# Optimization experiments

Hardware: AMD Instinct MI355X
Metric: run time of the kernel (lower is better)

Reference implementation:

```python
import jax, jax.numpy as jnp
import numpy as np

H = 16      # n_heads
HD = 48     # head_dim
D = H * HD  # d_model = 768
DZ = 128    # pair dim
EPS = 1e-5


def setup_inputs() -> dict:
    key = jax.random.key(0)
    ks = jax.random.split(key, 12)
    B, S = 1, 1024
    sc = 0.02
    return {
        "s": jax.random.normal(ks[0], (B, S, D), jnp.float32),
        "z": jax.random.normal(ks[1], (B, S, S, DZ), jnp.float32),
        "Wq": jax.random.normal(ks[2], (D, D), jnp.float32) * sc,
        "bq": jax.random.normal(ks[3], (D,), jnp.float32) * sc,
        "Wk": jax.random.normal(ks[4], (D, D), jnp.float32) * sc,
        "Wv": jax.random.normal(ks[5], (D, D), jnp.float32) * sc,
        "Wg": jax.random.normal(ks[6], (D, D), jnp.float32) * sc,
        "ln_w": jnp.ones((DZ,), jnp.float32),
        "ln_b": jnp.zeros((DZ,), jnp.float32),
        "Wz": jax.random.normal(ks[7], (H, DZ), jnp.float32) * sc,
        "Wo": jax.random.normal(ks[8], (D, D), jnp.float32) * sc,
    }


def reference(s, z, Wq, bq, Wk, Wv, Wg, ln_w, ln_b, Wz, Wo):
    B, S, _ = s.shape
    # fused QKV projection (q has bias; k, v do not)
    q = (s @ Wq.T + bq).reshape(B, S, H, HD).transpose(0, 2, 1, 3)  # [B,H,S,hd]
    k = (s @ Wk.T).reshape(B, S, H, HD).transpose(0, 2, 1, 3)
    v = (s @ Wv.T).reshape(B, S, H, HD).transpose(0, 2, 1, 3)
    # pair bias: LayerNorm(z) then Linear(DZ -> H), used as additive attn bias
    mu = jnp.mean(z, axis=-1, keepdims=True)
    var = jnp.mean(jnp.square(z - mu), axis=-1, keepdims=True)
    zn = (z - mu) * jax.lax.rsqrt(var + EPS) * ln_w + ln_b
    bias = jnp.einsum('bstc,hc->bhst', zn, Wz)  # [B,H,S,S]
    # scaled dot-product attention with pair bias
    scores = jnp.einsum('bhsd,bhtd->bhst', q, k) * (HD ** -0.5) + bias
    a = jax.nn.softmax(scores, axis=-1)
    o = jnp.einsum('bhst,bhtd->bhsd', a, v)           # [B,H,S,hd]
    o = o.transpose(0, 2, 1, 3).reshape(B, S, D)      # [B,S,D]
    # sigmoid gating and output projection
    g = s @ Wg.T
    o = o * jax.nn.sigmoid(g)
    return o @ Wo.T
```

## Files before the change

kernel.cpp:

```cpp
#include <hip/hip_runtime.h>

constexpr int H  = 16;
constexpr int HD = 48;
constexpr int D  = 768;
constexpr int DZ = 128;
constexpr int S  = 1024;
constexpr float EPS = 1e-5f;

typedef __attribute__((ext_vector_type(8))) short bf16x8;
typedef __attribute__((ext_vector_type(4))) float f32x4;

__device__ __forceinline__ float sigmoidf_(float x) { return 1.f / (1.f + __expf(-x)); }

__device__ __forceinline__ unsigned short f2b(float f) {
  unsigned u = __float_as_uint(f);
  u += 0x7FFFu + ((u >> 16) & 1u);
  return (unsigned short)(u >> 16);
}
__device__ __forceinline__ float b2f(unsigned short u) {
  return __uint_as_float((unsigned)u << 16);
}
__device__ __forceinline__ void split2(float x, unsigned short& h, unsigned short& l) {
  const unsigned short hb = f2b(x);
  const float hf = __uint_as_float((unsigned)hb << 16);
  h = hb;
  l = f2b(x - hf);
}
__device__ __forceinline__ unsigned pack2(unsigned short a, unsigned short b) {
  return (unsigned)a | ((unsigned)b << 16);
}

__global__ __launch_bounds__(256)
void prep_kernel(const float* __restrict__ s, const float* __restrict__ Wq,
                 const float* __restrict__ Wk, const float* __restrict__ Wv,
                 const float* __restrict__ Wg, const float* __restrict__ Wo,
                 unsigned short* __restrict__ s_hi,
                 unsigned short* __restrict__ w_hi, unsigned short* __restrict__ w_lo,
                 const float* __restrict__ Wz, const float* __restrict__ ln_w,
                 const float* __restrict__ ln_b, unsigned short* __restrict__ wzwb,
                 float* __restrict__ s12,
                 unsigned short* __restrict__ q_hi, unsigned short* __restrict__ k_hi) {
  if (blockIdx.x >= 769) {
    const int pid = (blockIdx.x - 769) * 6 + blockIdx.y;
    if (pid < 256) {
      const int i = pid * 256 + threadIdx.x;
      const int row = i >> 6, rem = i & 63;
      const int h = rem >> 2, off = (rem & 3) << 2;
      const size_t a = (size_t)row * 1024 + h * 64 + 48 + off;
      const ushort4 zz = {0, 0, 0, 0};
      *reinterpret_cast<ushort4*>(q_hi + a) = zz;
      *reinterpret_cast<ushort4*>(k_hi + a) = zz;
    }
    return;
  }
  if (blockIdx.x == 768) {
    if (blockIdx.y != 0) return;
    const int t = threadIdx.x;
    for (int e = t; e < 16 * DZ; e += 256) wzwb[e] = f2b(Wz[e] * ln_w[e & 127]);
    __syncthreads();
    if (t < 32) {
      const int h = t & 15;
      float a = 0.f;
      if (t < 16) {
        for (int c = 0; c < DZ; ++c) {
          const unsigned u = (unsigned)wzwb[h * DZ + c] << 16;
          a += __uint_as_float(u);
        }
      } else {
        for (int c = 0; c < DZ; ++c) a += Wz[h * DZ + c] * ln_b[c];
      }
      s12[t] = a;
    }
    return;
  }
  const int seg = blockIdx.y;
  const float* src;
  unsigned short* dh;
  unsigned short* dl = nullptr;
  int n;
  if (seg == 0) { src = s; dh = s_hi; n = S * D; }
  else {
    src = (seg == 1) ? Wq : (seg == 2) ? Wk : (seg == 3) ? Wv : (seg == 4) ? Wg : Wo;
    dh = w_hi + (size_t)(seg - 1) * D * D;
    if (seg == 5) dl = w_lo;
    n = D * D;
  }
  const int i4 = blockIdx.x * 256 + threadIdx.x;
  if (i4 * 4 < n) {
    const float4 v = *reinterpret_cast<const float4*>(src + (size_t)i4 * 4);
    ushort4 hh, ll;
    split2(v.x, hh.x, ll.x); split2(v.y, hh.y, ll.y);
    split2(v.z, hh.z, ll.z); split2(v.w, hh.w, ll.w);
    *reinterpret_cast<ushort4*>(dh + (size_t)i4 * 4) = hh;
    if (dl) *reinterpret_cast<ushort4*>(dl + (size_t)i4 * 4) = ll;
  }
}

__device__ __forceinline__ void mfma_core32_bf(const unsigned short* __restrict__ Ah,
                                               const unsigned short* __restrict__ Wh,
                                               const int m0, const int n0,
                                               const int k0, const int k1,
                                               f32x4& a00, f32x4& a01, f32x4& a10, f32x4& a11) {
  const int lane = threadIdx.x & 63;
  const int r16 = lane & 15, kg = lane >> 4;
  const unsigned short* pah = Ah + (size_t)(m0 + r16) * D + kg * 8;
  const unsigned short* pbh = Wh + (size_t)(n0 + r16) * D + kg * 8;
#pragma unroll 2
  for (int k = k0; k < k1; k += 32) {
    const bf16x8 ah0 = *reinterpret_cast<const bf16x8*>(pah + k);
    const bf16x8 ah1 = *reinterpret_cast<const bf16x8*>(pah + 16 * D + k);
    const bf16x8 bh0 = *reinterpret_cast<const bf16x8*>(pbh + k);
    const bf16x8 bh1 = *reinterpret_cast<const bf16x8*>(pbh + 16 * D + k);
    a00 = __builtin_amdgcn_mfma_f32_16x16x32_bf16(ah0, bh0, a00, 0, 0, 0);
    a01 = __builtin_amdgcn_mfma_f32_16x16x32_bf16(ah0, bh1, a01, 0, 0, 0);
    a10 = __builtin_amdgcn_mfma_f32_16x16x32_bf16(ah1, bh0, a10, 0, 0, 0);
    a11 = __builtin_amdgcn_mfma_f32_16x16x32_bf16(ah1, bh1, a11, 0, 0, 0);
  }
}

__global__ __launch_bounds__(256)
void qkvg_mfma_kernel(const unsigned short* __restrict__ s_hi,
                      const unsigned short* __restrict__ w_hi,
                      const float* __restrict__ bq,
                      unsigned short* __restrict__ q_hi,
                      unsigned short* __restrict__ k_hi,
                      unsigned short* __restrict__ vt_hi,
                      float* __restrict__ g_ws) {
  __shared__ float TT[4][32 * 33];
  __shared__ float CB[2][64][17];
  const int wv = threadIdx.x >> 6;
  const int pair = wv >> 1;
  const int khalf = wv & 1;
  const int tileid = blockIdx.x * 2 + pair;
  const int wsel = tileid / 768;
  const int rr = tileid % 768;
  const int m0 = (rr / 24) * 32, n0 = (rr % 24) * 32;
  f32x4 a00 = {0.f, 0.f, 0.f, 0.f}, a01 = a00, a10 = a00, a11 = a00;
  mfma_core32_bf(s_hi, w_hi + (size_t)wsel * D * D,
                 m0, n0, khalf * 384, khalf * 384 + 384, a00, a01, a10, a11);
  const int lane = threadIdx.x & 63;
  const int r16 = lane & 15, kg = lane >> 4;
  const float scale = 0.14433756729740643f;

  if (khalf == 1) {
#pragma unroll
    for (int r = 0; r < 4; ++r) {
      CB[pair][lane][r] = a00[r];
      CB[pair][lane][4 + r] = a01[r];
      CB[pair][lane][8 + r] = a10[r];
      CB[pair][lane][12 + r] = a11[r];
    }
  }
  __syncthreads();
  if (khalf == 1) return;
#pragma unroll
  for (int r = 0; r < 4; ++r) {
    a00[r] += CB[pair][lane][r];
    a01[r] += CB[pair][lane][4 + r];
    a10[r] += CB[pair][lane][8 + r];
    a11[r] += CB[pair][lane][12 + r];
  }

  float* T = TT[wv];
#pragma unroll
  for (int r = 0; r < 4; ++r) {
    T[(kg * 4 + r) * 33 + r16] = a00[r];
    T[(kg * 4 + r) * 33 + 16 + r16] = a01[r];
    T[(16 + kg * 4 + r) * 33 + r16] = a10[r];
    T[(16 + kg * 4 + r) * 33 + 16 + r16] = a11[r];
  }
  const int rr2 = lane >> 1, run = lane & 1;
  if (wsel <= 1) {
    const int row = m0 + rr2;
    const int col0 = n0 + run * 16;
    const int hcol0 = (col0 / 48) * 64 + (col0 % 48);
    unsigned short* dh = (wsel == 0) ? q_hi : k_hi;
#pragma unroll
    for (int p4 = 0; p4 < 4; ++p4) {
      float v0 = T[rr2 * 33 + run * 16 + p4 * 4 + 0];
      float v1 = T[rr2 * 33 + run * 16 + p4 * 4 + 1];
      float v2 = T[rr2 * 33 + run * 16 + p4 * 4 + 2];
      float v3 = T[rr2 * 33 + run * 16 + p4 * 4 + 3];
      if (wsel == 0) {
        v0 = (v0 + bq[col0 + p4 * 4 + 0]) * scale;
        v1 = (v1 + bq[col0 + p4 * 4 + 1]) * scale;
        v2 = (v2 + bq[col0 + p4 * 4 + 2]) * scale;
        v3 = (v3 + bq[col0 + p4 * 4 + 3]) * scale;
      }
      uint2 uh;
      uh.x = pack2(f2b(v0), f2b(v1)); uh.y = pack2(f2b(v2), f2b(v3));
      *reinterpret_cast<uint2*>(dh + (size_t)row * 1024 + hcol0 + p4 * 4) = uh;
    }
  } else if (wsel == 2) {
    const int c = lane >> 1;
    const int run2 = lane & 1;
    const int vc = n0 + c;
#pragma unroll
    for (int p4 = 0; p4 < 4; ++p4) {
      uint2 uh;
      uh.x = pack2(f2b(T[(run2 * 16 + p4 * 4 + 0) * 33 + c]),
                   f2b(T[(run2 * 16 + p4 * 4 + 1) * 33 + c]));
      uh.y = pack2(f2b(T[(run2 * 16 + p4 * 4 + 2) * 33 + c]),
                   f2b(T[(run2 * 16 + p4 * 4 + 3) * 33 + c]));
      *reinterpret_cast<uint2*>(vt_hi + (size_t)vc * 1024 + m0 + run2 * 16 + p4 * 4) = uh;
    }
  } else {
    const int row = m0 + rr2;
#pragma unroll
    for (int p4 = 0; p4 < 4; ++p4) {
      float4 v4;
      v4.x = T[rr2 * 33 + run * 16 + p4 * 4 + 0];
      v4.y = T[rr2 * 33 + run * 16 + p4 * 4 + 1];
      v4.z = T[rr2 * 33 + run * 16 + p4 * 4 + 2];
      v4.w = T[rr2 * 33 + run * 16 + p4 * 4 + 3];
      *reinterpret_cast<float4*>(g_ws + (size_t)row * D + n0 + run * 16 + p4 * 4) = v4;
    }
  }
}

__global__ __launch_bounds__(256)
void pair_bias_kernel(const float* __restrict__ z, const unsigned short* __restrict__ wzwb,
                      const float* __restrict__ s12, unsigned short* __restrict__ bias_out) {
  __shared__ float T[4][64 * 17];
  const int tid = threadIdx.x;
  const int lane = tid & 63;
  const int wv = tid >> 6;
  const int hq = lane & 15;
  const int grp = lane >> 4;

  bf16x8 bf[4];
#pragma unroll
  for (int m = 0; m < 4; ++m)
    bf[m] = *reinterpret_cast<const bf16x8*>(wzwb + hq * DZ + m * 32 + grp * 8);
  const float S1h = s12[hq], S2h = s12[16 + hq];

  const int chunk = blockIdx.x * 4 + wv;
  const size_t p0 = (size_t)chunk * 64;
  float* Tw = &T[wv][0];

#pragma unroll 1
  for (int sub = 0; sub < 4; ++sub) {
    const float* zr = z + (p0 + sub * 16 + hq) * DZ + grp * 8;
    f32x4 acc = {0.f, 0.f, 0.f, 0.f};
    float s1 = 0.f, s2 = 0.f;
#pragma unroll
    for (int m = 0; m < 4; ++m) {
      const float4 a0 = *reinterpret_cast<const float4*>(zr + m * 32);
      const float4 a1 = *reinterpret_cast<const float4*>(zr + m * 32 + 4);
      s1 += (a0.x + a0.y) + (a0.z + a0.w) + (a1.x + a1.y) + (a1.z + a1.w);
      s2 = fmaf(a0.x, a0.x, fmaf(a0.y, a0.y, fmaf(a0.z, a0.z, fmaf(a0.w, a0.w, s2))));
      s2 = fmaf(a1.x, a1.x, fmaf(a1.y, a1.y, fmaf(a1.z, a1.z, fmaf(a1.w, a1.w, s2))));
      bf16x8 af;
      af[0] = (short)f2b(a0.x); af[1] = (short)f2b(a0.y);
      af[2] = (short)f2b(a0.z); af[3] = (short)f2b(a0.w);
      af[4] = (short)f2b(a1.x); af[5] = (short)f2b(a1.y);
      af[6] = (short)f2b(a1.z); af[7] = (short)f2b(a1.w);
      acc = __builtin_amdgcn_mfma_f32_16x16x32_bf16(af, bf[m], acc, 0, 0, 0);
    }
    s1 += __shfl_xor(s1, 16); s1 += __shfl_xor(s1, 32);
    s2 += __shfl_xor(s2, 16); s2 += __shfl_xor(s2, 32);
    const float mu = s1 * (1.f / DZ);
    const float inv = rsqrtf(s2 * (1.f / DZ) - mu * mu + EPS);
#pragma unroll
    for (int r = 0; r < 4; ++r) {
      const int st = grp * 4 + r;
      const float mur = __shfl(mu, st);
      const float invr = __shfl(inv, st);
      Tw[(sub * 16 + st) * 17 + hq] = invr * (acc[r] - mur * S1h) + S2h;
    }
  }
#pragma unroll
  for (int hh = 0; hh < 16; ++hh)
    bias_out[(size_t)hh * S * S + p0 + lane] = f2b(Tw[lane * 17 + hh]);
}

constexpr int PST = 72;
constexpr int PRS = 52;

__global__ __launch_bounds__(256)
void attn_kernel(const unsigned short* __restrict__ q_hi,
                 const unsigned short* __restrict__ k_hi,
                 const unsigned short* __restrict__ vt_hi,
                 const unsigned short* __restrict__ bias, const float* __restrict__ g,
                 unsigned short* __restrict__ a_hi) {
  __shared__ unsigned short Ph[4][16 * PST];
  __shared__ float Pr[4][16 * PRS];
  const int lane = threadIdx.x & 63;
  const int wv = threadIdx.x >> 6;
  const int h = blockIdx.x >> 6;
  const int qb = blockIdx.x & 63;
  const int q0 = qb << 4;
  const int n16 = lane & 15, kg = lane >> 4;

  const size_t qbase = (size_t)(q0 + n16) * 1024 + h * 64;
  const bf16x8 qh0 = *reinterpret_cast<const bf16x8*>(q_hi + qbase + kg * 8);
  const bf16x8 qh1 = *reinterpret_cast<const bf16x8*>(q_hi + qbase + 32 + kg * 8);

  float mrow = -1e30f, lrow = 0.f;
  f32x4 accO[3] = {};
  unsigned short* php = Ph[wv];

#pragma unroll 1
  for (int t0 = wv * 256; t0 < wv * 256 + 256; t0 += 64) {
    f32x4 sc[4];
#pragma unroll
    for (int ts = 0; ts < 4; ++ts) {
      const size_t kb = (size_t)(t0 + ts * 16 + n16) * 1024 + h * 64;
      const bf16x8 kh0 = *reinterpret_cast<const bf16x8*>(k_hi + kb + kg * 8);
      const bf16x8 kh1 = *reinterpret_cast<const bf16x8*>(k_hi + kb + 32 + kg * 8);
      const ushort4 b4 = *reinterpret_cast<const ushort4*>(
          bias + (size_t)h * S * S + (size_t)(q0 + n16) * S + t0 + ts * 16 + kg * 4);
      f32x4 a;
      a[0] = b2f(b4.x); a[1] = b2f(b4.y); a[2] = b2f(b4.z); a[3] = b2f(b4.w);
      a = __builtin_amdgcn_mfma_f32_16x16x32_bf16(kh0, qh0, a, 0, 0, 0);
      a = __builtin_amdgcn_mfma_f32_16x16x32_bf16(kh1, qh1, a, 0, 0, 0);
      sc[ts] = a;
    }

    float tmax = sc[0][0];
#pragma unroll
    for (int ts = 0; ts < 4; ++ts)
#pragma unroll
      for (int r = 0; r < 4; ++r) tmax = fmaxf(tmax, sc[ts][r]);
    tmax = fmaxf(tmax, __shfl_xor(tmax, 16));
    tmax = fmaxf(tmax, __shfl_xor(tmax, 32));
    const float mn = fmaxf(mrow, tmax);
    const float fac = __expf(mrow - mn);
    mrow = mn;
    float psum = 0.f;
#pragma unroll
    for (int ts = 0; ts < 4; ++ts) {
      const float p0_ = __expf(sc[ts][0] - mn), p1_ = __expf(sc[ts][1] - mn);
      const float p2_ = __expf(sc[ts][2] - mn), p3_ = __expf(sc[ts][3] - mn);
      psum += (p0_ + p1_) + (p2_ + p3_);
      const int ti = ts * 16 + kg * 4;
      unsigned* wh = reinterpret_cast<unsigned*>(&php[n16 * PST + ti]);
      wh[0] = pack2(f2b(p0_), f2b(p1_));
      wh[1] = pack2(f2b(p2_), f2b(p3_));
    }
    lrow = lrow * fac + psum;

    float facr[4];
#pragma unroll
    for (int r = 0; r < 4; ++r) facr[r] = __shfl(fac, kg * 4 + r);
#pragma unroll
    for (int ds = 0; ds < 3; ++ds)
#pragma unroll
      for (int r = 0; r < 4; ++r) accO[ds][r] *= facr[r];

#pragma unroll
    for (int c = 0; c < 2; ++c) {
      const bf16x8 pah = *reinterpret_cast<const bf16x8*>(&php[n16 * PST + c * 32 + kg * 8]);
#pragma unroll
      for (int ds = 0; ds < 3; ++ds) {
        const size_t vb = (size_t)(h * 48 + ds * 16 + n16) * 1024 + t0 + c * 32 + kg * 8;
        const bf16x8 vh = *reinterpret_cast<const bf16x8*>(vt_hi + vb);
        accO[ds] = __builtin_amdgcn_mfma_f32_16x16x32_bf16(pah, vh, accO[ds], 0, 0, 0);
      }
    }
  }

  lrow += __shfl_xor(lrow, 16);
  lrow += __shfl_xor(lrow, 32);

  float* pw = Pr[wv];
#pragma unroll
  for (int ds = 0; ds < 3; ++ds)
#pragma unroll
    for (int r = 0; r < 4; ++r)
      pw[(kg * 4 + r) * PRS + ds * 16 + n16] = accO[ds][r];
  if (kg == 0) {
    pw[n16 * PRS + 48] = mrow;
    pw[n16 * PRS + 49] = lrow;
  }
  __syncthreads();

  const int row = threadIdx.x >> 4;
  const int dsub = threadIdx.x & 15;
  const float m0_ = Pr[0][row * PRS + 48], m1_ = Pr[1][row * PRS + 48];
  const float m2_ = Pr[2][row * PRS + 48], m3_ = Pr[3][row * PRS + 48];
  const float l0_ = Pr[0][row * PRS + 49], l1_ = Pr[1][row * PRS + 49];
  const float l2_ = Pr[2][row * PRS + 49], l3_ = Pr[3][row * PRS + 49];
  const float M = fmaxf(fmaxf(m0_, m1_), fmaxf(m2_, m3_));
  const float e0 = __expf(m0_ - M), e1 = __expf(m1_ - M);
  const float e2 = __expf(m2_ - M), e3 = __expf(m3_ - M);
  const float rl = 1.f / (l0_ * e0 + l1_ * e1 + l2_ * e2 + l3_ * e3);
#pragma unroll
  for (int j = 0; j < 3; ++j) {
    const int d = dsub * 3 + j;
    const float o = (Pr[0][row * PRS + d] * e0 + Pr[1][row * PRS + d] * e1 +
                     Pr[2][row * PRS + d] * e2 + Pr[3][row * PRS + d] * e3) * rl;
    const size_t idx = (size_t)(q0 + row) * D + h * 48 + d;
    const float a = o * sigmoidf_(g[idx]);
    a_hi[idx] = f2b(a);
  }
}

__global__ __launch_bounds__(256)
void outproj_mfma_kernel(const unsigned short* __restrict__ a_hi,
                         const unsigned short* __restrict__ wo_hi,
                         const unsigned short* __restrict__ wo_lo,
                         float* __restrict__ out) {
  __shared__ float CB[2][64][9];
  const int wv = threadIdx.x >> 6;
  const int pair = wv >> 1;
  const int khalf = wv & 1;
  const int tileid = blockIdx.x * 2 + pair;
  const int m0 = (tileid / 48) * 32, n0 = (tileid % 48) * 16;
  const int lane = threadIdx.x & 63;
  const int r16 = lane & 15, kg = lane >> 4;
  const unsigned short* pah = a_hi + (size_t)(m0 + r16) * D + kg * 8;
  const unsigned short* pbh = wo_hi + (size_t)(n0 + r16) * D + kg * 8;
  const unsigned short* pbl = wo_lo + (size_t)(n0 + r16) * D + kg * 8;
  f32x4 a0 = {0.f, 0.f, 0.f, 0.f}, a1 = a0;
#pragma unroll 2
  for (int k = khalf * 384; k < khalf * 384 + 384; k += 32) {
    const bf16x8 ah0 = *reinterpret_cast<const bf16x8*>(pah + k);
    const bf16x8 ah1 = *reinterpret_cast<const bf16x8*>(pah + 16 * D + k);
    const bf16x8 bh0 = *reinterpret_cast<const bf16x8*>(pbh + k);
    const bf16x8 bl0 = *reinterpret_cast<const bf16x8*>(pbl + k);
    a0 = __builtin_amdgcn_mfma_f32_16x16x32_bf16(ah0, bh0, a0, 0, 0, 0);
    a0 = __builtin_amdgcn_mfma_f32_16x16x32_bf16(ah0, bl0, a0, 0, 0, 0);
    a1 = __builtin_amdgcn_mfma_f32_16x16x32_bf16(ah1, bh0, a1, 0, 0, 0);
    a1 = __builtin_amdgcn_mfma_f32_16x16x32_bf16(ah1, bl0, a1, 0, 0, 0);
  }
  if (khalf == 1) {
#pragma unroll
    for (int r = 0; r < 4; ++r) {
      CB[pair][lane][r] = a0[r];
      CB[pair][lane][4 + r] = a1[r];
    }
  }
  __syncthreads();
  if (khalf == 1) return;
#pragma unroll
  for (int r = 0; r < 4; ++r) {
    a0[r] += CB[pair][lane][r];
    a1[r] += CB[pair][lane][4 + r];
  }
#pragma unroll
  for (int r = 0; r < 4; ++r) {
    out[(size_t)(m0 + kg * 4 + r) * D + n0 + r16] = a0[r];
    out[(size_t)(m0 + 16 + kg * 4 + r) * D + n0 + r16] = a1[r];
  }
}

extern "C" void kernel_launch(void* const* d_in, const int* in_sizes, int n_in,
                              void* d_out, int out_size, void* d_ws, size_t ws_size,
                              hipStream_t stream) {
  const float* s    = (const float*)d_in[0];
  const float* z    = (const float*)d_in[1];
  const float* Wq   = (const float*)d_in[2];
  const float* bq   = (const float*)d_in[3];
  const float* Wk   = (const float*)d_in[4];
  const float* Wv   = (const float*)d_in[5];
  const float* Wg   = (const float*)d_in[6];
  const float* ln_w = (const float*)d_in[7];
  const float* ln_b = (const float*)d_in[8];
  const float* Wz   = (const float*)d_in[9];
  const float* Wo   = (const float*)d_in[10];
  float* out = (float*)d_out;

  float* g_ws    = (float*)d_ws;
  float* s12_ws  = g_ws + (size_t)S * D;
  unsigned short* bias16 = (unsigned short*)(s12_ws + 32);
  unsigned short* wzwb_ws = bias16 + (size_t)H * S * S;
  unsigned short* s_hi = wzwb_ws + 2048;
  unsigned short* w_hi = s_hi + (size_t)S * D;
  unsigned short* wo_lo = w_hi + (size_t)5 * D * D;
  unsigned short* a_hi = wo_lo + (size_t)D * D;
  unsigned short* q_hi = a_hi + (size_t)S * D;
  unsigned short* k_hi = q_hi + (size_t)S * 1024;
  unsigned short* vt_hi = k_hi + (size_t)S * 1024;

  prep_kernel<<<dim3(812, 6), 256, 0, stream>>>(s, Wq, Wk, Wv, Wg, Wo,
                                                s_hi, w_hi, wo_lo,
                                                Wz, ln_w, ln_b, wzwb_ws, s12_ws,
                                                q_hi, k_hi);
  qkvg_mfma_kernel<<<1536, 256, 0, stream>>>(s_hi, w_hi, bq,
                                             q_hi, k_hi, vt_hi, g_ws);
  pair_bias_kernel<<<4096, 256, 0, stream>>>(z, wzwb_ws, s12_ws, bias16);
  attn_kernel<<<1024, 256, 0, stream>>>(q_hi, k_hi, vt_hi,
                                        bias16, g_ws, a_hi);
  outproj_mfma_kernel<<<768, 256, 0, stream>>>(a_hi, w_hi + (size_t)4 * D * D,
                                               wo_lo, out);
}
```

Before: 221.8 us.

## Split attention key range across eight waves instead of four

Each attention block now uses 512 threads (8 waves), and each wave handles 128 keys instead of 256. The per-wave partial softmax states are merged across 8 partitions in shared memory by the first 256 threads. This aims to raise parallelism and latency hiding in the attention kernel. The cost is a larger merge step, more shared memory per block, and idle threads during the final combine.

```diff
diff --git a/kernel.cpp b/kernel.cpp
--- a/kernel.cpp
+++ b/kernel.cpp
@@ -275,16 +275,16 @@
 }
 
 constexpr int PST = 72;
-constexpr int PRS = 52;
-
-__global__ __launch_bounds__(256)
+constexpr int PRS = 50;
+
+__global__ __launch_bounds__(512)
 void attn_kernel(const unsigned short* __restrict__ q_hi,
                  const unsigned short* __restrict__ k_hi,
                  const unsigned short* __restrict__ vt_hi,
                  const unsigned short* __restrict__ bias, const float* __restrict__ g,
                  unsigned short* __restrict__ a_hi) {
-  __shared__ unsigned short Ph[4][16 * PST];
-  __shared__ float Pr[4][16 * PRS];
+  __shared__ unsigned short Ph[8][16 * PST];
+  __shared__ float Pr[8][16 * PRS];
   const int lane = threadIdx.x & 63;
   const int wv = threadIdx.x >> 6;
   const int h = blockIdx.x >> 6;
@@ -301,7 +301,7 @@
   unsigned short* php = Ph[wv];
 
 #pragma unroll 1
-  for (int t0 = wv * 256; t0 < wv * 256 + 256; t0 += 64) {
+  for (int t0 = wv * 128; t0 < wv * 128 + 128; t0 += 64) {
     f32x4 sc[4];
 #pragma unroll
     for (int ts = 0; ts < 4; ++ts) {
@@ -375,24 +375,37 @@
   }
   __syncthreads();
 
-  const int row = threadIdx.x >> 4;
-  const int dsub = threadIdx.x & 15;
-  const float m0_ = Pr[0][row * PRS + 48], m1_ = Pr[1][row * PRS + 48];
-  const float m2_ = Pr[2][row * PRS + 48], m3_ = Pr[3][row * PRS + 48];
-  const float l0_ = Pr[0][row * PRS + 49], l1_ = Pr[1][row * PRS + 49];
-  const float l2_ = Pr[2][row * PRS + 49], l3_ = Pr[3][row * PRS + 49];
-  const float M = fmaxf(fmaxf(m0_, m1_), fmaxf(m2_, m3_));
-  const float e0 = __expf(m0_ - M), e1 = __expf(m1_ - M);
-  const float e2 = __expf(m2_ - M), e3 = __expf(m3_ - M);
-  const float rl = 1.f / (l0_ * e0 + l1_ * e1 + l2_ * e2 + l3_ * e3);
-#pragma unroll
-  for (int j = 0; j < 3; ++j) {
-    const int d = dsub * 3 + j;
-    const float o = (Pr[0][row * PRS + d] * e0 + Pr[1][row * PRS + d] * e1 +
-                     Pr[2][row * PRS + d] * e2 + Pr[3][row * PRS + d] * e3) * rl;
-    const size_t idx = (size_t)(q0 + row) * D + h * 48 + d;
-    const float a = o * sigmoidf_(g[idx]);
-    a_hi[idx] = f2b(a);
+  if (threadIdx.x < 256) {
+    const int row = threadIdx.x >> 4;
+    const int dsub = threadIdx.x & 15;
+    float mp[8], lp[8];
+#pragma unroll
+    for (int p = 0; p < 8; ++p) {
+      mp[p] = Pr[p][row * PRS + 48];
+      lp[p] = Pr[p][row * PRS + 49];
+    }
+    float M = mp[0];
+#pragma unroll
+    for (int p = 1; p < 8; ++p) M = fmaxf(M, mp[p]);
+    float ep[8];
+    float denom = 0.f;
+#pragma unroll
+    for (int p = 0; p < 8; ++p) {
+      ep[p] = __expf(mp[p] - M);
+      denom += lp[p] * ep[p];
+    }
+    const float rl = 1.f / denom;
+#pragma unroll
+    for (int j = 0; j < 3; ++j) {
+      const int d = dsub * 3 + j;
+      float o = 0.f;
+#pragma unroll
+      for (int p = 0; p < 8; ++p) o += Pr[p][row * PRS + d] * ep[p];
+      o *= rl;
+      const size_t idx = (size_t)(q0 + row) * D + h * 48 + d;
+      const float a = o * sigmoidf_(g[idx]);
+      a_hi[idx] = f2b(a);
+    }
   }
 }
 
@@ -480,7 +493,7 @@
   qkvg_mfma_kernel<<<1536, 256, 0, stream>>>(s_hi, w_hi, bq,
                                              q_hi, k_hi, vt_hi, g_ws);
   pair_bias_kernel<<<4096, 256, 0, stream>>>(z, wzwb_ws, s12_ws, bias16);
-  attn_kernel<<<1024, 256, 0, stream>>>(q_hi, k_hi, vt_hi,
+  attn_kernel<<<1024, 512, 0, stream>>>(q_hi, k_hi, vt_hi,
                                         bias16, g_ws, a_hi);
   outproj_mfma_kernel<<<768, 256, 0, stream>>>(a_hi, w_hi + (size_t)4 * D * D,
                                                wo_lo, out);
```

New measurement: 224.5 us. No clear change (+1.2%).
